# Kernel tuning notes

Measured on AMD Instinct MI355X. Metric: run time of the kernel, lower is better.

## Reference

```python
import jax, jax.numpy as jnp
import numpy as np

HEADS = 16
LN_EPS = 1e-5


def _layernorm(x, w, b):
    mu = jnp.mean(x, axis=-1, keepdims=True)
    var = jnp.mean(jnp.square(x - mu), axis=-1, keepdims=True)
    return (x - mu) * jax.lax.rsqrt(var + LN_EPS) * w + b


def setup_inputs() -> dict:
    key = jax.random.key(0)
    ks = jax.random.split(key, 14)
    B, L, E, HID = 4, 4096, 1024, 4096
    s = 0.02
    return {
        "x": jax.random.normal(ks[0], (B, L, E), dtype=jnp.float32),
        "w_q": jax.random.normal(ks[1], (E, E), dtype=jnp.float32) * s,
        "w_k": jax.random.normal(ks[2], (E, E), dtype=jnp.float32) * s,
        "w_v": jax.random.normal(ks[3], (E, E), dtype=jnp.float32) * s,
        "w_o": jax.random.normal(ks[4], (E, E), dtype=jnp.float32) * s,
        "b_o": jnp.zeros((E,), dtype=jnp.float32),
        "ln1_w": jnp.ones((E,), dtype=jnp.float32),
        "ln1_b": jnp.zeros((E,), dtype=jnp.float32),
        "ln2_w": jnp.ones((E,), dtype=jnp.float32),
        "ln2_b": jnp.zeros((E,), dtype=jnp.float32),
        "w_ff1": jax.random.normal(ks[5], (E, HID), dtype=jnp.float32) * s,
        "b_ff1": jnp.zeros((HID,), dtype=jnp.float32),
        "w_ff2": jax.random.normal(ks[6], (HID, E), dtype=jnp.float32) * s,
        "b_ff2": jnp.zeros((E,), dtype=jnp.float32),
    }


def reference(x, w_q, w_k, w_v, w_o, b_o, ln1_w, ln1_b, ln2_w, ln2_b,
              w_ff1, b_ff1, w_ff2, b_ff2):
    N, L, E = x.shape
    H = HEADS
    D = E // H
    # projections -> (N, H, L, D) exactly as the torch view+permute
    q = (x @ w_q).reshape(N, L, H, D).transpose(0, 2, 1, 3)
    k = (x @ w_k).reshape(N, L, H, D).transpose(0, 2, 1, 3)
    v = (x @ w_v).reshape(N, L, H, D).transpose(0, 2, 1, 3)
    # Faithful to source: einsum subscripts applied to the PERMUTED tensors,
    # so 'q'/'k' bind to the heads axis and 'h','d' contract over (length, head_dim).
    # energy: (N, H, H)
    energy = jnp.einsum('nqhd,nkhd->nqk', q, k)
    attention = jax.nn.softmax(energy / (float(E) ** 0.5), axis=2)
    # 'k' and 'v' are independent sum indices -> out[n,q,h,d] = (sum_k att) * (sum_v v)
    out = jnp.einsum('nqk,nvhd->nqhd', attention, v)  # (N, H, L, D)
    out = out.reshape(N, L, H * D)  # row-major flatten, same as torch .reshape
    attn_out = out @ w_o + b_o
    # residual + LayerNorm (dropout is identity in eval)
    h1 = _layernorm(attn_out + x, ln1_w, ln1_b)
    ff = jax.nn.relu(h1 @ w_ff1 + b_ff1) @ w_ff2 + b_ff2
    return _layernorm(ff + h1, ln2_w, ln2_b)
```

## Files before the change

kernel.cpp:

```cpp
#include <hip/hip_runtime.h>
#include <stdint.h>
#include <stddef.h>

typedef __bf16 bf16_t;
typedef __bf16 bf16x8 __attribute__((ext_vector_type(8)));
typedef __bf16 bf16x4 __attribute__((ext_vector_type(4)));
typedef float f32x4 __attribute__((ext_vector_type(4)));

#define E_DIM 1024
#define HID_DIM 4096
#define NROWS 16384

__device__ __forceinline__ void async16(const bf16_t* g, void* l) {
    __builtin_amdgcn_global_load_lds(
        (const __attribute__((address_space(1))) void*)g,
        (__attribute__((address_space(3))) void*)l,
        16, 0, 0);
}

__global__ void detect_dtype(const unsigned int* __restrict__ ln1_w_raw, int* __restrict__ flag) {
    if (threadIdx.x == 0) {
        *flag = (ln1_w_raw[0] == 0x3F800000u) ? 0 : 1;
    }
}

__device__ __forceinline__ float load_in(const void* p, size_t idx, int isb) {
    if (isb) return (float)((const bf16_t*)p)[idx];
    return ((const float*)p)[idx];
}

struct VecArgs {
    const void* p[7];
    float* o[7];
    int n[7];
};

__global__ __launch_bounds__(256) void convert_vecs(VecArgs a, const int* __restrict__ dflag) {
    int isb = *dflag;
    int seg = blockIdx.y;
    int i = blockIdx.x * 256 + threadIdx.x;
    if (i < a.n[seg]) a.o[seg][i] = load_in(a.p[seg], (size_t)i, isb);
}

__global__ __launch_bounds__(256) void convert_x(const void* __restrict__ in, bf16_t* __restrict__ out,
                                                 const int* __restrict__ dflag) {
    int isb = *dflag;
    size_t i = ((size_t)blockIdx.x * 256 + threadIdx.x) * 8;
    if (isb) {
        *(bf16x8*)(out + i) = *((const bf16x8*)((const bf16_t*)in + i));
    } else {
        const float* f = (const float*)in + i;
        bf16x8 v;
#pragma unroll
        for (int j = 0; j < 8; j++) v[j] = (bf16_t)f[j];
        *(bf16x8*)(out + i) = v;
    }
}

__global__ void transpose_to_bf16(const void* __restrict__ in, bf16_t* __restrict__ out,
                                  int R, int C, const int* __restrict__ dflag) {
    int isb = *dflag;
    __shared__ bf16_t tile[32][33];
    int c0 = blockIdx.x * 32, r0 = blockIdx.y * 32;
    int tx = threadIdx.x, ty = threadIdx.y;
#pragma unroll
    for (int i = 0; i < 32; i += 8)
        tile[ty + i][tx] = (bf16_t)load_in(in, (size_t)(r0 + ty + i) * C + (c0 + tx), isb);
    __syncthreads();
#pragma unroll
    for (int i = 0; i < 32; i += 8)
        out[(size_t)(c0 + ty + i) * R + (r0 + tx)] = tile[tx][ty + i];
}

__global__ void fold_wv(const void* __restrict__ w_v, bf16_t* __restrict__ w_vs_t,
                        const int* __restrict__ dflag) {
    int isb = *dflag;
    int d = threadIdx.x;
    int e = blockIdx.x;
    float s = 0.f;
#pragma unroll
    for (int i = 0; i < 16; i++)
        s += load_in(w_v, (size_t)e * 1024 + i * 64 + d, isb);
    w_vs_t[((size_t)d << 10) + e] = (bf16_t)s;
}

template <int BM, int BN, int SWZ_G, bool RELU, bool OUT_BF16, bool HAS_BIAS>
__global__ __launch_bounds__(256) void gemm_bt(const bf16_t* __restrict__ A,
                                               const bf16_t* __restrict__ Bt,
                                               const float* __restrict__ bias,
                                               void* __restrict__ Cv,
                                               int M, int N, int K) {
    constexpr int BK = 64;
    constexpr int WM = BM / 2;
    constexpr int WN = BN / 2;
    constexpr int TM = WM / 16;
    constexpr int TN = WN / 16;
    __shared__ __align__(16) bf16_t As[BM][BK];
    __shared__ __align__(16) bf16_t Bs[BN][BK];

    const int tid = threadIdx.x;
    const int lane = tid & 63;
    const int wid = tid >> 6;
    const int wr = wid >> 1, wc = wid & 1;
    const int lm = lane & 15, quad = lane >> 4;
    const int lm7 = lm & 7;

    int bx = blockIdx.x, by = blockIdx.y;
    if (SWZ_G > 0) {
        const int flat = by * gridDim.x + bx;
        const int S = SWZ_G * gridDim.x;
        const int g = flat / S, r = flat % S;
        bx = r / SWZ_G;
        by = g * SWZ_G + (r % SWZ_G);
    }
    const int bm = by * BM, bn = bx * BN;

    const int rsub = lane >> 3;
    const int csub = ((lane & 7) ^ rsub) << 3;

    f32x4 acc[TM][TN];
#pragma unroll
    for (int i = 0; i < TM; i++)
#pragma unroll
        for (int j = 0; j < TN; j++) acc[i][j] = (f32x4){0.f, 0.f, 0.f, 0.f};

    const bf16_t* Ap = A + (size_t)bm * K + csub;
    const bf16_t* Bp = Bt + (size_t)bn * K + csub;

    for (int k0 = 0; k0 < K; k0 += BK) {
#pragma unroll
        for (int cc = 0; cc < BM / 32; cc++) {
            const int c = cc * 4 + wid;
            async16(Ap + (size_t)(c * 8 + rsub) * K + k0, (char*)&As[0][0] + c * 1024);
        }
#pragma unroll
        for (int cc = 0; cc < BN / 32; cc++) {
            const int c = cc * 4 + wid;
            async16(Bp + (size_t)(c * 8 + rsub) * K + k0, (char*)&Bs[0][0] + c * 1024);
        }
        __syncthreads();

#pragma unroll
        for (int kk = 0; kk < 2; kk++) {
            bf16x8 af[TM], bfr[TN];
#pragma unroll
            for (int i = 0; i < TM; i++) {
                const int row = wr * WM + i * 16 + lm;
                const int pb = ((kk * 4 + quad) ^ lm7) << 3;
                af[i] = *(const bf16x8*)(&As[row][pb]);
            }
#pragma unroll
            for (int j = 0; j < TN; j++) {
                const int row = wc * WN + j * 16 + lm;
                const int pb = ((kk * 4 + quad) ^ lm7) << 3;
                bfr[j] = *(const bf16x8*)(&Bs[row][pb]);
            }
#pragma unroll
            for (int i = 0; i < TM; i++)
#pragma unroll
                for (int j = 0; j < TN; j++)
                    acc[i][j] = __builtin_amdgcn_mfma_f32_16x16x32_bf16(af[i], bfr[j], acc[i][j], 0, 0, 0);
        }
        __syncthreads();
    }

    const int gm0 = bm + wr * WM, gn0 = bn + wc * WN;
#pragma unroll
    for (int i = 0; i < TM; i++) {
#pragma unroll
        for (int j = 0; j < TN; j++) {
            const int col = gn0 + j * 16 + lm;
            float bv = HAS_BIAS ? bias[col] : 0.f;
#pragma unroll
            for (int r = 0; r < 4; r++) {
                const int row = gm0 + i * 16 + quad * 4 + r;
                float v = acc[i][j][r] + bv;
                if (RELU) v = fmaxf(v, 0.f);
                if (OUT_BF16)
                    ((bf16_t*)Cv)[(size_t)row * N + col] = (bf16_t)v;
                else
                    ((float*)Cv)[(size_t)row * N + col] = v;
            }
        }
    }
}

template <int SWZ_G, bool RELU, bool OUT_BF16, bool HAS_BIAS>
__global__ __launch_bounds__(512, 2) void gemm256(const bf16_t* __restrict__ A,
                                                  const bf16_t* __restrict__ Bt,
                                                  const float* __restrict__ bias,
                                                  void* __restrict__ Cv,
                                                  int M, int N, int K) {
    constexpr int BK = 64;
    __shared__ __align__(16) bf16_t As[2][256][BK];
    __shared__ __align__(16) bf16_t Bs[2][256][BK];

    const int tid = threadIdx.x;
    const int lane = tid & 63;
    const int wid = tid >> 6;
    const int wr = wid >> 2;
    const int wc = wid & 3;
    const int lm = lane & 15, quad = lane >> 4;
    const int lm7 = lm & 7;
    const int rsub = lane >> 3;
    const int csub = ((lane & 7) ^ rsub) << 3;

    int bx = blockIdx.x, by = blockIdx.y;
    if (SWZ_G > 0) {
        const int flat = by * gridDim.x + bx;
        const int S = SWZ_G * gridDim.x;
        const int g = flat / S, r = flat % S;
        bx = r / SWZ_G;
        by = g * SWZ_G + (r % SWZ_G);
    }
    const int bm = by * 256, bn = bx * 256;

    const bf16_t* Ap = A + (size_t)bm * K + csub;
    const bf16_t* Bp = Bt + (size_t)bn * K + csub;
    const int c0 = wid * 2;

#define STAGE_A(b, h, kt) do { \
        const size_t ko = (size_t)(kt) * BK; \
        async16(Ap + (size_t)((h) * 128 + c0 * 8 + rsub) * K + ko, \
                (char*)(&As[(b)][0][0]) + (h) * 16384 + c0 * 1024); \
        async16(Ap + (size_t)((h) * 128 + (c0 + 1) * 8 + rsub) * K + ko, \
                (char*)(&As[(b)][0][0]) + (h) * 16384 + (c0 + 1) * 1024); \
    } while (0)
#define STAGE_B(b, h, kt) do { \
        const size_t ko = (size_t)(kt) * BK; \
        async16(Bp + (size_t)((h) * 128 + c0 * 8 + rsub) * K + ko, \
                (char*)(&Bs[(b)][0][0]) + (h) * 16384 + c0 * 1024); \
        async16(Bp + (size_t)((h) * 128 + (c0 + 1) * 8 + rsub) * K + ko, \
                (char*)(&Bs[(b)][0][0]) + (h) * 16384 + (c0 + 1) * 1024); \
    } while (0)
#define FENCE_BARRIER() do { \
        asm volatile("" ::: "memory"); \
        __builtin_amdgcn_s_barrier(); \
        asm volatile("" ::: "memory"); \
    } while (0)

    f32x4 acc[8][4];
#pragma unroll
    for (int i = 0; i < 8; i++)
#pragma unroll
        for (int j = 0; j < 4; j++) acc[i][j] = (f32x4){0.f, 0.f, 0.f, 0.f};

    auto ldA = [&](int b, int im, int kk) -> bf16x8 {
        const int row = wr * 128 + im * 16 + lm;
        const int pb = ((kk * 4 + quad) ^ lm7) << 3;
        return *(const bf16x8*)(&As[b][row][pb]);
    };
    auto ldB = [&](int b, int jn, int kk) -> bf16x8 {
        const int row = wc * 64 + jn * 16 + lm;
        const int pb = ((kk * 4 + quad) ^ lm7) << 3;
        return *(const bf16x8*)(&Bs[b][row][pb]);
    };

    const int nt = K / BK;

    STAGE_A(0, 0, 0); STAGE_A(0, 1, 0);
    STAGE_B(0, 0, 0); STAGE_B(0, 1, 0);
    if (nt > 1) {
        STAGE_A(1, 0, 1); STAGE_A(1, 1, 1);
        STAGE_B(1, 0, 1); STAGE_B(1, 1, 1);
        asm volatile("s_waitcnt vmcnt(8)" ::: "memory");
    } else {
        asm volatile("s_waitcnt vmcnt(0)" ::: "memory");
    }
    __builtin_amdgcn_s_barrier();
    asm volatile("" ::: "memory");

    bf16x8 afA[4], afB[4], b01[2][2], b23[2][2];
    for (int t = 0; t < nt; ++t) {
        const int cur = t & 1;
        const bool pf = (t + 2 < nt);

#pragma unroll
        for (int i = 0; i < 4; ++i) afA[i] = ldA(cur, i, 0);
#pragma unroll
        for (int j = 0; j < 2; ++j) b01[j][0] = ldB(cur, j, 0);
#pragma unroll
        for (int i = 0; i < 4; ++i) afB[i] = ldA(cur, i, 1);
#pragma unroll
        for (int j = 0; j < 2; ++j) b01[j][1] = ldB(cur, j, 1);
#pragma unroll
        for (int j = 0; j < 2; ++j) b23[j][0] = ldB(cur, 2 + j, 0);
#pragma unroll
        for (int j = 0; j < 2; ++j) b23[j][1] = ldB(cur, 2 + j, 1);
        __builtin_amdgcn_s_setprio(1);
#pragma unroll
        for (int i = 0; i < 4; ++i)
#pragma unroll
            for (int j = 0; j < 2; ++j) {
                acc[i][j] = __builtin_amdgcn_mfma_f32_16x16x32_bf16(afA[i], b01[j][0], acc[i][j], 0, 0, 0);
                acc[i][j] = __builtin_amdgcn_mfma_f32_16x16x32_bf16(afB[i], b01[j][1], acc[i][j], 0, 0, 0);
            }
#pragma unroll
        for (int i = 0; i < 4; ++i)
#pragma unroll
            for (int j = 0; j < 2; ++j) {
                acc[i][2 + j] = __builtin_amdgcn_mfma_f32_16x16x32_bf16(afA[i], b23[j][0], acc[i][2 + j], 0, 0, 0);
                acc[i][2 + j] = __builtin_amdgcn_mfma_f32_16x16x32_bf16(afB[i], b23[j][1], acc[i][2 + j], 0, 0, 0);
            }
        __builtin_amdgcn_s_setprio(0);
#pragma unroll
        for (int i = 0; i < 4; ++i) afA[i] = ldA(cur, 4 + i, 0);
        FENCE_BARRIER();

#pragma unroll
        for (int i = 0; i < 4; ++i) afB[i] = ldA(cur, 4 + i, 1);
        if (pf) { STAGE_B(cur, 0, t + 2); STAGE_B(cur, 1, t + 2); }
        __builtin_amdgcn_s_setprio(1);
#pragma unroll
        for (int i = 0; i < 4; ++i)
#pragma unroll
            for (int j = 0; j < 2; ++j) {
                acc[4 + i][2 + j] = __builtin_amdgcn_mfma_f32_16x16x32_bf16(afA[i], b23[j][0], acc[4 + i][2 + j], 0, 0, 0);
                acc[4 + i][2 + j] = __builtin_amdgcn_mfma_f32_16x16x32_bf16(afB[i], b23[j][1], acc[4 + i][2 + j], 0, 0, 0);
            }
        __builtin_amdgcn_s_setprio(0);
        FENCE_BARRIER();

        if (pf) { STAGE_A(cur, 0, t + 2); STAGE_A(cur, 1, t + 2); }
        __builtin_amdgcn_s_setprio(1);
#pragma unroll
        for (int i = 0; i < 4; ++i)
#pragma unroll
            for (int j = 0; j < 2; ++j) {
                acc[4 + i][j] = __builtin_amdgcn_mfma_f32_16x16x32_bf16(afA[i], b01[j][0], acc[4 + i][j], 0, 0, 0);
                acc[4 + i][j] = __builtin_amdgcn_mfma_f32_16x16x32_bf16(afB[i], b01[j][1], acc[4 + i][j], 0, 0, 0);
            }
        __builtin_amdgcn_s_setprio(0);
        if (pf) {
            asm volatile("s_waitcnt vmcnt(8)" ::: "memory");
        } else {
            asm volatile("s_waitcnt vmcnt(0)" ::: "memory");
        }
        FENCE_BARRIER();
    }
#undef STAGE_A
#undef STAGE_B
#undef FENCE_BARRIER

    const int gm0 = bm + wr * 128, gn0 = bn + wc * 64;
#pragma unroll
    for (int i = 0; i < 8; i++) {
#pragma unroll
        for (int j = 0; j < 4; j++) {
            const int col = gn0 + j * 16 + lm;
            float bv = HAS_BIAS ? bias[col] : 0.f;
#pragma unroll
            for (int r = 0; r < 4; r++) {
                const int row = gm0 + i * 16 + quad * 4 + r;
                float v = acc[i][j][r] + bv;
                if (RELU) v = fmaxf(v, 0.f);
                if (OUT_BF16)
                    ((bf16_t*)Cv)[(size_t)row * N + col] = (bf16_t)v;
                else
                    ((float*)Cv)[(size_t)row * N + col] = v;
            }
        }
    }
}

__device__ __forceinline__ void block_reduce2(float& s, float& s2, float* red, int tid) {
#pragma unroll
    for (int o = 32; o > 0; o >>= 1) {
        s += __shfl_down(s, o, 64);
        s2 += __shfl_down(s2, o, 64);
    }
    const int wid = tid >> 6;
    if ((tid & 63) == 0) { red[wid] = s; red[4 + wid] = s2; }
    __syncthreads();
    s = red[0] + red[1] + red[2] + red[3];
    s2 = red[4] + red[5] + red[6] + red[7];
}

__global__ __launch_bounds__(256) void ln1_fused(const float* __restrict__ attn,
                                                 const bf16_t* __restrict__ xbf,
                                                 const float* __restrict__ w,
                                                 const float* __restrict__ b,
                                                 bf16_t* __restrict__ h1) {
    const int row = blockIdx.x;
    const int n = row >> 12;
    const int lp = row & 4095;
    const float* arow = attn + (((size_t)(n << 8) + (lp & 255)) << 10);
    const bf16_t* xrow = xbf + ((size_t)row << 10);
    const int tid = threadIdx.x;
    const int c4 = tid << 2;
    __shared__ float red[8];
    f32x4 a = *(const f32x4*)(arow + c4);
    bf16x4 xv = *(const bf16x4*)(xrow + c4);
    float v[4];
    float s = 0.f, s2 = 0.f;
#pragma unroll
    for (int u = 0; u < 4; u++) {
        float val = a[u] + (float)xv[u];
        v[u] = val; s += val; s2 += val * val;
    }
    block_reduce2(s, s2, red, tid);
    const float mu = s * (1.f / 1024.f);
    const float var = s2 * (1.f / 1024.f) - mu * mu;
    const float rstd = rsqrtf(var + 1e-5f);
    f32x4 wv = *(const f32x4*)(w + c4);
    f32x4 bv = *(const f32x4*)(b + c4);
    bf16x4 hv;
#pragma unroll
    for (int u = 0; u < 4; u++)
        hv[u] = (bf16_t)((v[u] - mu) * rstd * wv[u] + bv[u]);
    *(bf16x4*)(h1 + ((size_t)row << 10) + c4) = hv;
}

__global__ __launch_bounds__(256) void ln2_fused(const bf16_t* __restrict__ ff,
                                                 const bf16_t* __restrict__ h1,
                                                 const float* __restrict__ w,
                                                 const float* __restrict__ b,
                                                 void* __restrict__ outp,
                                                 const int* __restrict__ dflag,
                                                 int row0) {
    const int isb = *dflag;
    const int row = blockIdx.x;
    const int tid = threadIdx.x;
    const int c4 = tid << 2;
    __shared__ float red[8];
    bf16x4 fv = *(const bf16x4*)(ff + ((size_t)row << 10) + c4);
    bf16x4 hv = *(const bf16x4*)(h1 + ((size_t)row << 10) + c4);
    float v[4];
    float s = 0.f, s2 = 0.f;
#pragma unroll
    for (int u = 0; u < 4; u++) {
        float val = (float)fv[u] + (float)hv[u];
        v[u] = val; s += val; s2 += val * val;
    }
    block_reduce2(s, s2, red, tid);
    const float mu = s * (1.f / 1024.f);
    const float var = s2 * (1.f / 1024.f) - mu * mu;
    const float rstd = rsqrtf(var + 1e-5f);
    f32x4 wv = *(const f32x4*)(w + c4);
    f32x4 bv = *(const f32x4*)(b + c4);
    const size_t base = ((size_t)(row0 + row) << 10) + c4;
    if (isb) {
        bf16x4 ov;
#pragma unroll
        for (int u = 0; u < 4; u++) ov[u] = (bf16_t)((v[u] - mu) * rstd * wv[u] + bv[u]);
        *(bf16x4*)((bf16_t*)outp + base) = ov;
    } else {
        f32x4 ov;
#pragma unroll
        for (int u = 0; u < 4; u++) ov[u] = (v[u] - mu) * rstd * wv[u] + bv[u];
        *(f32x4*)((float*)outp + base) = ov;
    }
}

extern "C" void kernel_launch(void* const* d_in, const int* in_sizes, int n_in,
                              void* d_out, int out_size, void* d_ws, size_t ws_size,
                              hipStream_t stream) {
    char* ws = (char*)d_ws;
    const size_t MB = 1u << 20;

    int*    dflag   = (int*)ws;
    float*  vec0    = (float*)(ws + 4096);
    float*  vec_b_o   = vec0 + 0 * 4096;
    float*  vec_bff1  = vec0 + 1 * 4096;
    float*  vec_bff2  = vec0 + 2 * 4096;
    float*  vec_ln1w  = vec0 + 3 * 4096;
    float*  vec_ln1b  = vec0 + 4 * 4096;
    float*  vec_ln2w  = vec0 + 5 * 4096;
    float*  vec_ln2b  = vec0 + 6 * 4096;
    bf16_t* w_vs_t  = (bf16_t*)(ws + 256 * 1024);
    bf16_t* w_o_t   = (bf16_t*)(ws + 1 * MB);
    bf16_t* w_ff1_t = (bf16_t*)(ws + 3 * MB);
    bf16_t* w_ff2_t = (bf16_t*)(ws + 11 * MB);
    bf16_t* vsum    = (bf16_t*)(ws + 19 * MB);
    float*  attn    = (float*)(ws + 21 * MB);
    bf16_t* xbf     = (bf16_t*)(ws + 25 * MB);
    bf16_t* h1      = (bf16_t*)(ws + 57 * MB);
    bf16_t* hidden  = (bf16_t*)(ws + 89 * MB);

    int chunk;
    if (ws_size >= 250 * MB)      chunk = 16384;
    else if (ws_size >= 170 * MB) chunk = 8192;
    else                          chunk = 4096;
    bf16_t* ffbuf = (bf16_t*)(ws + 89 * MB + (size_t)chunk * HID_DIM * sizeof(bf16_t));

    detect_dtype<<<1, 64, 0, stream>>>((const unsigned int*)d_in[6], dflag);

    VecArgs va;
    va.p[0] = d_in[5];  va.o[0] = vec_b_o;  va.n[0] = 1024;
    va.p[1] = d_in[11]; va.o[1] = vec_bff1; va.n[1] = 4096;
    va.p[2] = d_in[13]; va.o[2] = vec_bff2; va.n[2] = 1024;
    va.p[3] = d_in[6];  va.o[3] = vec_ln1w; va.n[3] = 1024;
    va.p[4] = d_in[7];  va.o[4] = vec_ln1b; va.n[4] = 1024;
    va.p[5] = d_in[8];  va.o[5] = vec_ln2w; va.n[5] = 1024;
    va.p[6] = d_in[9];  va.o[6] = vec_ln2b; va.n[6] = 1024;
    convert_vecs<<<dim3(16, 7), 256, 0, stream>>>(va, dflag);

    convert_x<<<8192, 256, 0, stream>>>(d_in[0], xbf, dflag);

    transpose_to_bf16<<<dim3(32, 32),  dim3(32, 8), 0, stream>>>(d_in[4],  w_o_t,   1024, 1024, dflag);
    transpose_to_bf16<<<dim3(128, 32), dim3(32, 8), 0, stream>>>(d_in[10], w_ff1_t, 1024, 4096, dflag);
    transpose_to_bf16<<<dim3(32, 128), dim3(32, 8), 0, stream>>>(d_in[12], w_ff2_t, 4096, 1024, dflag);
    fold_wv<<<1024, 64, 0, stream>>>(d_in[3], w_vs_t, dflag);

    gemm_bt<64, 64, 0, false, true, false><<<dim3(1, 256), 256, 0, stream>>>(
        xbf, w_vs_t, nullptr, vsum, NROWS, 64, E_DIM);

    gemm_bt<128, 128, 0, false, false, true><<<dim3(8, 8), 256, 0, stream>>>(
        vsum, w_o_t, vec_b_o, attn, 1024, 1024, 1024);

    ln1_fused<<<NROWS, 256, 0, stream>>>(attn, xbf, vec_ln1w, vec_ln1b, h1);

    for (int r0 = 0; r0 < NROWS; r0 += chunk) {
        const bf16_t* h1c = h1 + (size_t)r0 * E_DIM;
        gemm256<16, true, true, true><<<dim3(HID_DIM / 256, chunk / 256), 512, 0, stream>>>(
            h1c, w_ff1_t, vec_bff1, hidden, chunk, HID_DIM, E_DIM);
        gemm256<16, false, true, true><<<dim3(E_DIM / 256, chunk / 256), 512, 0, stream>>>(
            hidden, w_ff2_t, vec_bff2, ffbuf, chunk, E_DIM, HID_DIM);
        ln2_fused<<<chunk, 256, 0, stream>>>(ffbuf, h1c, vec_ln2w, vec_ln2b, d_out, dflag, r0);
    }
}
```

Measured before the change: 549.8 us.

## Software-pipeline LDS fragment loads across GEMM iterations with explicit waitcnts

Restructures the bf16 MFMA GEMM main loop so that the A and B0/B1 register fragments for the next k-tile are read from the other LDS buffer at the end of each iteration. The remaining fragment reads are placed between MFMA groups, with explicit lgkmcnt waits and sched_barriers so the compiler keeps this interleaving. The intent is to hide LDS read latency behind MFMA work. In exchange, the global-load wait changes from vmcnt(8) at the end of the iteration to vmcnt(0) in the middle, which may reduce overlap of global-to-LDS transfers. The nt>1 guard is also removed, so the code now assumes at least two k-tiles.

```diff
diff --git a/kernel.cpp b/kernel.cpp
--- a/kernel.cpp
+++ b/kernel.cpp
@@ -238,6 +238,7 @@
         __builtin_amdgcn_s_barrier(); \
         asm volatile("" ::: "memory"); \
     } while (0)
+#define MFMA_BF16(a, b, c) __builtin_amdgcn_mfma_f32_16x16x32_bf16((a), (b), (c), 0, 0, 0)
 
     f32x4 acc[8][4];
 #pragma unroll
@@ -260,87 +261,89 @@
 
     STAGE_A(0, 0, 0); STAGE_A(0, 1, 0);
     STAGE_B(0, 0, 0); STAGE_B(0, 1, 0);
-    if (nt > 1) {
-        STAGE_A(1, 0, 1); STAGE_A(1, 1, 1);
-        STAGE_B(1, 0, 1); STAGE_B(1, 1, 1);
-        asm volatile("s_waitcnt vmcnt(8)" ::: "memory");
-    } else {
-        asm volatile("s_waitcnt vmcnt(0)" ::: "memory");
-    }
+    STAGE_A(1, 0, 1); STAGE_A(1, 1, 1);
+    STAGE_B(1, 0, 1); STAGE_B(1, 1, 1);
+    asm volatile("s_waitcnt vmcnt(8)" ::: "memory");
     __builtin_amdgcn_s_barrier();
     asm volatile("" ::: "memory");
 
     bf16x8 afA[4], afB[4], b01[2][2], b23[2][2];
+#pragma unroll
+    for (int i = 0; i < 4; ++i) { afA[i] = ldA(0, i, 0); afB[i] = ldA(0, i, 1); }
+#pragma unroll
+    for (int j = 0; j < 2; ++j) { b01[j][0] = ldB(0, j, 0); b01[j][1] = ldB(0, j, 1); }
+
     for (int t = 0; t < nt; ++t) {
-        const int cur = t & 1;
+        const int cur = t & 1, nxt = cur ^ 1;
         const bool pf = (t + 2 < nt);
 
-#pragma unroll
-        for (int i = 0; i < 4; ++i) afA[i] = ldA(cur, i, 0);
-#pragma unroll
-        for (int j = 0; j < 2; ++j) b01[j][0] = ldB(cur, j, 0);
-#pragma unroll
-        for (int i = 0; i < 4; ++i) afB[i] = ldA(cur, i, 1);
-#pragma unroll
-        for (int j = 0; j < 2; ++j) b01[j][1] = ldB(cur, j, 1);
-#pragma unroll
-        for (int j = 0; j < 2; ++j) b23[j][0] = ldB(cur, 2 + j, 0);
-#pragma unroll
-        for (int j = 0; j < 2; ++j) b23[j][1] = ldB(cur, 2 + j, 1);
+        asm volatile("s_waitcnt lgkmcnt(0)" ::: "memory");
+        __builtin_amdgcn_sched_barrier(0);
         __builtin_amdgcn_s_setprio(1);
 #pragma unroll
         for (int i = 0; i < 4; ++i)
 #pragma unroll
             for (int j = 0; j < 2; ++j) {
-                acc[i][j] = __builtin_amdgcn_mfma_f32_16x16x32_bf16(afA[i], b01[j][0], acc[i][j], 0, 0, 0);
-                acc[i][j] = __builtin_amdgcn_mfma_f32_16x16x32_bf16(afB[i], b01[j][1], acc[i][j], 0, 0, 0);
-            }
+                acc[i][j] = MFMA_BF16(afA[i], b01[j][0], acc[i][j]);
+                acc[i][j] = MFMA_BF16(afB[i], b01[j][1], acc[i][j]);
+            }
+        __builtin_amdgcn_s_setprio(0);
+#pragma unroll
+        for (int j = 0; j < 2; ++j) { b23[j][0] = ldB(cur, 2 + j, 0); b23[j][1] = ldB(cur, 2 + j, 1); }
+        FENCE_BARRIER();
+
+        asm volatile("s_waitcnt lgkmcnt(0)" ::: "memory");
+        __builtin_amdgcn_sched_barrier(0);
+        __builtin_amdgcn_s_setprio(1);
 #pragma unroll
         for (int i = 0; i < 4; ++i)
 #pragma unroll
             for (int j = 0; j < 2; ++j) {
-                acc[i][2 + j] = __builtin_amdgcn_mfma_f32_16x16x32_bf16(afA[i], b23[j][0], acc[i][2 + j], 0, 0, 0);
-                acc[i][2 + j] = __builtin_amdgcn_mfma_f32_16x16x32_bf16(afB[i], b23[j][1], acc[i][2 + j], 0, 0, 0);
+                acc[i][2 + j] = MFMA_BF16(afA[i], b23[j][0], acc[i][2 + j]);
+                acc[i][2 + j] = MFMA_BF16(afB[i], b23[j][1], acc[i][2 + j]);
             }
         __builtin_amdgcn_s_setprio(0);
 #pragma unroll
-        for (int i = 0; i < 4; ++i) afA[i] = ldA(cur, 4 + i, 0);
+        for (int i = 0; i < 4; ++i) { afA[i] = ldA(cur, 4 + i, 0); afB[i] = ldA(cur, 4 + i, 1); }
+        asm volatile("s_waitcnt vmcnt(0)" ::: "memory");
         FENCE_BARRIER();
 
-#pragma unroll
-        for (int i = 0; i < 4; ++i) afB[i] = ldA(cur, 4 + i, 1);
         if (pf) { STAGE_B(cur, 0, t + 2); STAGE_B(cur, 1, t + 2); }
+        asm volatile("s_waitcnt lgkmcnt(0)" ::: "memory");
+        __builtin_amdgcn_sched_barrier(0);
         __builtin_amdgcn_s_setprio(1);
 #pragma unroll
         for (int i = 0; i < 4; ++i)
 #pragma unroll
             for (int j = 0; j < 2; ++j) {
-                acc[4 + i][2 + j] = __builtin_amdgcn_mfma_f32_16x16x32_bf16(afA[i], b23[j][0], acc[4 + i][2 + j], 0, 0, 0);
-                acc[4 + i][2 + j] = __builtin_amdgcn_mfma_f32_16x16x32_bf16(afB[i], b23[j][1], acc[4 + i][2 + j], 0, 0, 0);
+                acc[4 + i][2 + j] = MFMA_BF16(afA[i], b23[j][0], acc[4 + i][2 + j]);
+                acc[4 + i][2 + j] = MFMA_BF16(afB[i], b23[j][1], acc[4 + i][2 + j]);
             }
         __builtin_amdgcn_s_setprio(0);
         FENCE_BARRIER();
 
         if (pf) { STAGE_A(cur, 0, t + 2); STAGE_A(cur, 1, t + 2); }
+        __builtin_amdgcn_sched_barrier(0);
         __builtin_amdgcn_s_setprio(1);
 #pragma unroll
         for (int i = 0; i < 4; ++i)
 #pragma unroll
             for (int j = 0; j < 2; ++j) {
-                acc[4 + i][j] = __builtin_amdgcn_mfma_f32_16x16x32_bf16(afA[i], b01[j][0], acc[4 + i][j], 0, 0, 0);
-                acc[4 + i][j] = __builtin_amdgcn_mfma_f32_16x16x32_bf16(afB[i], b01[j][1], acc[4 + i][j], 0, 0, 0);
+                acc[4 + i][j] = MFMA_BF16(afA[i], b01[j][0], acc[4 + i][j]);
+                acc[4 + i][j] = MFMA_BF16(afB[i], b01[j][1], acc[4 + i][j]);
             }
         __builtin_amdgcn_s_setprio(0);
-        if (pf) {
-            asm volatile("s_waitcnt vmcnt(8)" ::: "memory");
-        } else {
-            asm volatile("s_waitcnt vmcnt(0)" ::: "memory");
-        }
+#pragma unroll
+        for (int i = 0; i < 4; ++i) { afA[i] = ldA(nxt, i, 0); afB[i] = ldA(nxt, i, 1); }
+#pragma unroll
+        for (int j = 0; j < 2; ++j) { b01[j][0] = ldB(nxt, j, 0); b01[j][1] = ldB(nxt, j, 1); }
         FENCE_BARRIER();
     }
+    asm volatile("s_waitcnt vmcnt(0) lgkmcnt(0)" ::: "memory");
 #undef STAGE_A
 #undef STAGE_B
 #undef FENCE_BARRIER
+#undef MFMA_BF16
 
     const int gm0 = bm + wr * 128, gn0 = bn + wc * 64;
 #pragma unroll
```

Result: faster. 512.7 us (-6.7%).
